# Kernel tuning notes

Measured on AMD Instinct MI355X. Metric: run time of the kernel, lower is better.

## Reference

```python
import jax, jax.numpy as jnp
import numpy as np

N_NODES = 100000
N_EDGES = 1600000
N_GRAPHS = 1000
NODES_PER_GRAPH = 100
D_IN = 128
D_HID = 128
N_TASKS = 12


def setup_inputs() -> dict:
    key = jax.random.key(0)
    ks = jax.random.split(key, 6)
    X = jax.random.normal(ks[0], (N_NODES, D_IN), dtype=jnp.float32)
    edge_index = jax.random.randint(ks[1], (2, N_EDGES), 0, N_NODES, dtype=jnp.int64)
    graph_sizes = jnp.full((N_GRAPHS,), NODES_PER_GRAPH, dtype=jnp.int64)  # sums to N_NODES
    s0 = (2.0 / D_IN) ** 0.5
    W0 = jax.random.normal(ks[2], (D_IN, D_HID), dtype=jnp.float32) * s0
    b0 = jnp.zeros((D_HID,), dtype=jnp.float32)
    W1 = jax.random.normal(ks[3], (D_HID, D_HID), dtype=jnp.float32) * s0
    b1 = jnp.zeros((D_HID,), dtype=jnp.float32)
    Wf = jax.random.normal(ks[4], (D_HID, N_TASKS), dtype=jnp.float32) * s0
    bf = jnp.zeros((N_TASKS,), dtype=jnp.float32)
    return {"X": X, "edge_index": edge_index, "graph_sizes": graph_sizes,
            "W0": W0, "b0": b0, "W1": W1, "b1": b1, "Wf": Wf, "bf": bf}


def reference(X, edge_index, graph_sizes, W0, b0, W1, b1, Wf, bf):
    src, dst = edge_index[0], edge_index[1]
    n = X.shape[0]

    def gconv(x, W, b):
        # GCN-style message passing with self term: sum_{j->i} (x_j W) + x_i W + b
        xw = x @ W                                                    # [N, d]
        agg = jax.ops.segment_sum(xw[src], dst, num_segments=n)       # [N, d]
        return agg + xw + b

    # stacked conv -> relu -> dropout(eval=identity)
    h = jax.nn.relu(gconv(X, W0, b0))
    h = jax.nn.relu(gconv(h, W1, b1))
    out = jax.nn.sigmoid(h @ Wf + bf)                                  # [N, T]

    # ragged per-graph mean readout as a single segment-mean
    g = graph_sizes.shape[0]
    seg_ids = jnp.repeat(jnp.arange(g), graph_sizes, total_repeat_length=n)
    sums = jax.ops.segment_sum(out, seg_ids, num_segments=g)           # [G, T]
    return sums / graph_sizes[:, None].astype(out.dtype)
```

## Files before the change

kernel.cpp:

```cpp
#include <hip/hip_runtime.h>
#include <math.h>

#define D 128
#define NBUCK_MAX 1024
#define PER       2048
#define NCHUNK_PAD 1024
#define CAPB      4096
#define CAPE      2600

typedef unsigned short u16;
typedef unsigned int   u32;
typedef __attribute__((ext_vector_type(8))) short short8;
typedef __attribute__((ext_vector_type(4))) float f32x4;
typedef __attribute__((ext_vector_type(2))) float f32x2;

static __device__ __forceinline__ u16 f32_to_bf16(float f) {
    u32 u = __builtin_bit_cast(u32, f);
    u32 r = (u + 0x7FFFu + ((u >> 16) & 1u)) >> 16;
    return (u16)r;
}
static __device__ __forceinline__ u32 pack_bf16x2(float lo, float hi) {
    return (u32)f32_to_bf16(lo) | ((u32)f32_to_bf16(hi) << 16);
}
static __device__ __forceinline__ float bf16lo_to_f32(u32 v) {
    return __builtin_bit_cast(float, v << 16);
}
static __device__ __forceinline__ float bf16hi_to_f32(u32 v) {
    return __builtin_bit_cast(float, v & 0xFFFF0000u);
}

__global__ __launch_bounds__(256) void prep_place(const int* __restrict__ src, const int* __restrict__ dst,
                                                  int E, int nbuck, int nchunk,
                                                  u32* __restrict__ edgeBuf, u16* __restrict__ offTab,
                                                  const float* __restrict__ W0, const float* __restrict__ W1,
                                                  u16* __restrict__ Wp0, u16* __restrict__ Wp1,
                                                  const float* __restrict__ Wf, float* __restrict__ Wfp,
                                                  const int* __restrict__ gsz, int G, int* __restrict__ goff) {
    const int b = blockIdx.x;
    const int tid = threadIdx.x;
    if (b < nchunk) {
        __shared__ int cnt[NBUCK_MAX];
        __shared__ u32 pay[PER];
        for (int i = tid; i < nbuck; i += 256) cnt[i] = 0;
        __syncthreads();
        const int s = b * PER, e = min(E, s + PER);
        int dv[8];
        #pragma unroll
        for (int k = 0; k < 8; k++) {
            int i = s + tid + k * 256;
            dv[k] = (i < e) ? dst[i] : -1;
            if (dv[k] >= 0) atomicAdd(&cnt[dv[k] >> 7], 1);
        }
        __syncthreads();
        if (tid < 64) {
            int carry = 0;
            int rounds = (nbuck + 63) >> 6;
            for (int r = 0; r < rounds; r++) {
                int i = r * 64 + tid;
                int v = (i < nbuck) ? cnt[i] : 0;
                int incl = v;
                #pragma unroll
                for (int off = 1; off < 64; off <<= 1) { int t = __shfl_up(incl, off); if (tid >= off) incl += t; }
                int excl = carry + incl - v;
                if (i < nbuck) { offTab[(size_t)i * NCHUNK_PAD + b] = (u16)excl; cnt[i] = excl; }
                carry += __shfl(incl, 63);
            }
            if (tid == 0) offTab[(size_t)nbuck * NCHUNK_PAD + b] = (u16)carry;
        }
        __syncthreads();
        #pragma unroll
        for (int k = 0; k < 8; k++) {
            int i = s + tid + k * 256;
            if (i < e) {
                int pos = atomicAdd(&cnt[dv[k] >> 7], 1);
                pay[pos] = (u32)src[i] | ((u32)(dv[k] & 127) << 20);
            }
        }
        __syncthreads();
        const int m = e - s;
        for (int i = tid; i < m; i += 256) edgeBuf[(size_t)b * PER + i] = pay[i];
    } else if (b == nchunk) {
        __shared__ int wsum[8];
        int base = tid * 4;
        int v[4];
        #pragma unroll
        for (int k = 0; k < 4; k++) v[k] = (base + k < G) ? gsz[base + k] : 0;
        int s = v[0] + v[1] + v[2] + v[3];
        int lane = tid & 63;
        int incl = s;
        #pragma unroll
        for (int off = 1; off < 64; off <<= 1) { int t = __shfl_up(incl, off); if (lane >= off) incl += t; }
        int wv = tid >> 6;
        if (lane == 63) wsum[wv] = incl;
        __syncthreads();
        int woff = 0;
        for (int w = 0; w < wv; w++) woff += wsum[w];
        int run = woff + incl - s;
        #pragma unroll
        for (int k = 0; k < 4; k++) {
            if (base + k <= G) goff[base + k] = run;
            run += v[k];
        }
    } else if (b == nchunk + 1) {
        for (int i = tid; i < 64 * 24; i += 256) {
            int lane = i / 24, r = i % 24, k = r / 3, j = r % 3;
            Wfp[i] = Wf[(((lane & 15) * 8) + k) * 12 + 3 * (lane >> 4) + j];
        }
    } else {
        int gidx = (b - (nchunk + 2)) * 256 + tid;
        const float* W = (gidx < 128 * 128) ? W0 : W1;
        u16* Wp = (gidx < 128 * 128) ? Wp0 : Wp1;
        int idx = gidx & (128 * 128 - 1);
        int j = idx & 7, lane = (idx >> 3) & 63, kt = (idx >> 9) & 3, nt = idx >> 11;
        int k = kt * 32 + ((lane >> 4) << 3) + j;
        int n = nt * 16 + (lane & 15);
        Wp[idx] = f32_to_bf16(W[k * 128 + n]);
    }
}

static __device__ __forceinline__ void gemm_body(const short8 af[4], const u16* __restrict__ Wp,
                                                 u16* __restrict__ outb, int N, int row0,
                                                 int tid, int wave, int lane, int quad, int l16,
                                                 u16* Cs) {
    f32x4 acc[8];
    #pragma unroll
    for (int nt = 0; nt < 8; nt++) acc[nt] = (f32x4){0.f, 0.f, 0.f, 0.f};
    #pragma unroll
    for (int kt = 0; kt < 4; kt++) {
        #pragma unroll
        for (int nt = 0; nt < 8; nt++) {
            short8 bf = *(const short8*)(Wp + ((size_t)(nt * 4 + kt) * 64 + lane) * 8);
            acc[nt] = __builtin_amdgcn_mfma_f32_16x16x32_bf16(af[kt], bf, acc[nt], 0, 0, 0);
        }
    }
    #pragma unroll
    for (int nt = 0; nt < 8; nt++) {
        #pragma unroll
        for (int r = 0; r < 4; r++) {
            int rl = wave * 16 + quad * 4 + r;
            Cs[rl * 136 + nt * 16 + l16] = f32_to_bf16(acc[nt][r]);
        }
    }
    __syncthreads();
    for (int i = tid; i < 64 * 16; i += 256) {
        int row = i >> 4, chunk = i & 15;
        int grow = row0 + row;
        if (grow <= N)
            *(uint4*)(outb + (size_t)grow * 128 + chunk * 8) =
                *(const uint4*)(Cs + row * 136 + chunk * 8);
    }
}

__global__ __launch_bounds__(256) void finalize_gemm0(const u32* __restrict__ edgeBuf,
                                                      const u16* __restrict__ offTab,
                                                      int2* __restrict__ rowse, int* __restrict__ col_idx,
                                                      int nbuck, int nchunk,
                                                      const float* __restrict__ A, const u16* __restrict__ Wp,
                                                      u16* __restrict__ outb, int N) {
    __shared__ int sbuf[7680];
    const int tid = threadIdx.x;
    if ((int)blockIdx.x < nbuck) {
        u32* eL     = (u32*)sbuf;
        int* sorted = sbuf + CAPE;
        int* hist   = sbuf + 2 * CAPE + 128;
        int* lcur   = sbuf + 2 * CAPE + 256;
        int* scnt   = sbuf + 2 * CAPE + 384;
        int* sbase  = sbuf + 2 * CAPE + 1408;
        const int b = blockIdx.x;
        for (int c = tid; c < NCHUNK_PAD; c += 256) {
            if (c < nchunk) {
                int off0 = offTab[(size_t)b * NCHUNK_PAD + c];
                int off1 = offTab[(size_t)(b + 1) * NCHUNK_PAD + c];
                scnt[c] = (off0 << 16) | (off1 - off0);
            } else scnt[c] = 0;
        }
        if (tid < 128) hist[tid] = 0;
        __syncthreads();
        if (tid < 64) {
            int carry = 0;
            #pragma unroll
            for (int c4 = 0; c4 < NCHUNK_PAD / 64; c4++) {
                int v = scnt[c4 * 64 + tid] & 0xFFFF;
                int incl = v;
                #pragma unroll
                for (int off = 1; off < 64; off <<= 1) { int t = __shfl_up(incl, off); if (tid >= off) incl += t; }
                sbase[c4 * 64 + tid] = carry + incl - v;
                carry += __shfl(incl, 63);
            }
            if (tid == 0) sbase[NCHUNK_PAD] = carry;
        }
        __syncthreads();
        const int nE = min(sbase[NCHUNK_PAD], CAPE);
        for (int p = tid; p < nE; p += 256) {
            int lo = 0, hi = NCHUNK_PAD;
            #pragma unroll
            for (int s = 0; s < 10; s++) {
                int mid = (lo + hi) >> 1;
                if (sbase[mid] <= p) lo = mid; else hi = mid;
            }
            int rec = scnt[lo];
            eL[p] = edgeBuf[(size_t)lo * PER + (rec >> 16) + (p - sbase[lo])];
        }
        __syncthreads();
        for (int i = tid; i < nE; i += 256)
            atomicAdd(&hist[(int)(eL[i] >> 20)], 1);
        __syncthreads();
        if (tid < 64) {
            int v0 = hist[tid * 2], v1 = hist[tid * 2 + 1];
            int s = v0 + v1;
            int incl = s;
            #pragma unroll
            for (int off = 1; off < 64; off <<= 1) { int t = __shfl_up(incl, off); if (tid >= off) incl += t; }
            int excl = incl - s;
            int le0 = excl + tid * 2;
            int le1 = le0 + v0 + 1;
            lcur[tid * 2]     = le0 + 1;
            lcur[tid * 2 + 1] = le1 + 1;
            int node = b * 128 + tid * 2;
            int st0 = b * CAPB + le0, st1 = b * CAPB + le1;
            if (node < N)     { rowse[node]     = make_int2(st0, st1);          sorted[le0] = node; }
            if (node + 1 < N) { rowse[node + 1] = make_int2(st1, st1 + v1 + 1); sorted[le1] = node + 1; }
        }
        __syncthreads();
        for (int i = tid; i < nE; i += 256) {
            u32 p = eL[i];
            int pos = atomicAdd(&lcur[p >> 20], 1);
            sorted[pos] = (int)(p & 0xFFFFFu);
        }
        __syncthreads();
        const int nTot = nE + min(128, N - b * 128);
        for (int i = tid; i < nTot; i += 256)
            col_idx[b * CAPB + i] = sorted[i];
    } else {
        u16* Cs = (u16*)sbuf;
        const int bid = blockIdx.x - nbuck;
        const int wave = tid >> 6, lane = tid & 63, quad = lane >> 4, l16 = lane & 15;
        const int row0 = bid * 64;
        const int arow = row0 + wave * 16 + l16;
        union { u32 u[4]; short8 s; } cv;
        short8 af[4];
        if (arow < N) {
            const float* ab = A + (size_t)arow * 128 + quad * 8;
            #pragma unroll
            for (int kt = 0; kt < 4; kt++) {
                float4 x0 = *(const float4*)(ab + kt * 32);
                float4 x1 = *(const float4*)(ab + kt * 32 + 4);
                cv.u[0] = pack_bf16x2(x0.x, x0.y);
                cv.u[1] = pack_bf16x2(x0.z, x0.w);
                cv.u[2] = pack_bf16x2(x1.x, x1.y);
                cv.u[3] = pack_bf16x2(x1.z, x1.w);
                af[kt] = cv.s;
            }
        } else {
            short8 z = {0, 0, 0, 0, 0, 0, 0, 0};
            #pragma unroll
            for (int kt = 0; kt < 4; kt++) af[kt] = z;
        }
        gemm_body(af, Wp, outb, N, row0, tid, wave, lane, quad, l16, Cs);
    }
}

static __device__ __forceinline__ void add_row(f32x2* acc, uint4 u) {
    acc[0] += (f32x2){bf16lo_to_f32(u.x), bf16hi_to_f32(u.x)};
    acc[1] += (f32x2){bf16lo_to_f32(u.y), bf16hi_to_f32(u.y)};
    acc[2] += (f32x2){bf16lo_to_f32(u.z), bf16hi_to_f32(u.z)};
    acc[3] += (f32x2){bf16lo_to_f32(u.w), bf16hi_to_f32(u.w)};
}

static __device__ __forceinline__ void gather2(const u16* __restrict__ xwb, const int2* __restrict__ rowse,
                                               const int* __restrict__ col_idx, const float* __restrict__ bias,
                                               int wid0, int wid1, int lane, int N, int q, int d8,
                                               float r0[8], float r1[8]) {
    f32x2 accA[4], accB[4];
    #pragma unroll
    for (int t = 0; t < 4; t++) { accA[t] = (f32x2){0.f, 0.f}; accB[t] = (f32x2){0.f, 0.f}; }
    int2 seA = rowse[wid0];
    int2 seB = rowse[wid1];
    int ia = seA.x + lane, ib = seB.x + lane;
    int jA = (ia < seA.y) ? col_idx[ia] : N;
    int jB = (ib < seB.y) ? col_idx[ib] : N;
    int cntA = __builtin_amdgcn_readfirstlane(min(64, seA.y - seA.x));
    int cntB = __builtin_amdgcn_readfirstlane(min(64, seB.y - seB.x));
    int mx = max(cntA, cntB);
    for (int i = 0; i < mx; i += 8) {
        uint4 ra0, ra1, rb0, rb1;
        const bool dA = i < cntA, dB = i < cntB;
        if (dA) {
            int a0 = __shfl(jA, i + q);
            int a1 = __shfl(jA, i + 4 + q);
            ra0 = *(const uint4*)(xwb + (size_t)a0 * D + d8);
            ra1 = *(const uint4*)(xwb + (size_t)a1 * D + d8);
        }
        if (dB) {
            int b0 = __shfl(jB, i + q);
            int b1 = __shfl(jB, i + 4 + q);
            rb0 = *(const uint4*)(xwb + (size_t)b0 * D + d8);
            rb1 = *(const uint4*)(xwb + (size_t)b1 * D + d8);
        }
        if (dA) { add_row(accA, ra0); add_row(accA, ra1); }
        if (dB) { add_row(accB, rb0); add_row(accB, rb1); }
    }
    for (int e = seA.x + 64; e < seA.y; e += 64) {
        int idx = e + lane;
        int j = (idx < seA.y) ? col_idx[idx] : N;
        int cnt = min(64, seA.y - e);
        for (int i = 0; i < cnt; i += 8) {
            int j0 = __shfl(j, i + q);
            int j1 = __shfl(j, i + 4 + q);
            add_row(accA, *(const uint4*)(xwb + (size_t)j0 * D + d8));
            add_row(accA, *(const uint4*)(xwb + (size_t)j1 * D + d8));
        }
    }
    for (int e = seB.x + 64; e < seB.y; e += 64) {
        int idx = e + lane;
        int j = (idx < seB.y) ? col_idx[idx] : N;
        int cnt = min(64, seB.y - e);
        for (int i = 0; i < cnt; i += 8) {
            int j0 = __shfl(j, i + q);
            int j1 = __shfl(j, i + 4 + q);
            add_row(accB, *(const uint4*)(xwb + (size_t)j0 * D + d8));
            add_row(accB, *(const uint4*)(xwb + (size_t)j1 * D + d8));
        }
    }

    float av0[8] = {accA[0].x, accA[0].y, accA[1].x, accA[1].y, accA[2].x, accA[2].y, accA[3].x, accA[3].y};
    float av1[8] = {accB[0].x, accB[0].y, accB[1].x, accB[1].y, accB[2].x, accB[2].y, accB[3].x, accB[3].y};
    #pragma unroll
    for (int t = 0; t < 8; t++) {
        av0[t] += __shfl_xor(av0[t], 16);
        av0[t] += __shfl_xor(av0[t], 32);
        av1[t] += __shfl_xor(av1[t], 16);
        av1[t] += __shfl_xor(av1[t], 32);
    }
    float4 ba = *(const float4*)(bias + d8);
    float4 bb = *(const float4*)(bias + d8 + 4);
    r0[0] = fmaxf(av0[0] + ba.x, 0.f);
    r0[1] = fmaxf(av0[1] + ba.y, 0.f);
    r0[2] = fmaxf(av0[2] + ba.z, 0.f);
    r0[3] = fmaxf(av0[3] + ba.w, 0.f);
    r0[4] = fmaxf(av0[4] + bb.x, 0.f);
    r0[5] = fmaxf(av0[5] + bb.y, 0.f);
    r0[6] = fmaxf(av0[6] + bb.z, 0.f);
    r0[7] = fmaxf(av0[7] + bb.w, 0.f);
    r1[0] = fmaxf(av1[0] + ba.x, 0.f);
    r1[1] = fmaxf(av1[1] + ba.y, 0.f);
    r1[2] = fmaxf(av1[2] + ba.z, 0.f);
    r1[3] = fmaxf(av1[3] + ba.w, 0.f);
    r1[4] = fmaxf(av1[4] + bb.x, 0.f);
    r1[5] = fmaxf(av1[5] + bb.y, 0.f);
    r1[6] = fmaxf(av1[6] + bb.z, 0.f);
    r1[7] = fmaxf(av1[7] + bb.w, 0.f);
}

__global__ __launch_bounds__(256) void agg_gemm1(const u16* __restrict__ xwb, const int2* __restrict__ rowse,
                                                 const int* __restrict__ col_idx, const float* __restrict__ bias,
                                                 const u16* __restrict__ Wp, u16* __restrict__ outb, int N) {
    __shared__ u16 hs[16 * 136];
    __shared__ u16 Cs[16 * 136];
    const int tid = threadIdx.x;
    const int wave = tid >> 6, lane = tid & 63, quad = lane >> 4, l16 = lane & 15;
    const int tile = blockIdx.x * 16;
    const int d8 = l16 * 8;
    #pragma unroll
    for (int m = 0; m < 4; m += 2) {
        int nl0 = wave * 4 + m, nl1 = nl0 + 1;
        int wid0 = tile + nl0, wid1 = tile + nl1;
        float r0[8], r1[8];
        int g0 = min(wid0, N - 1), g1 = min(wid1, N - 1);
        gather2(xwb, rowse, col_idx, bias, g0, g1, lane, N, quad, d8, r0, r1);
        if (quad == 0) {
            uint4 o0, o1;
            if (wid0 < N) {
                o0.x = pack_bf16x2(r0[0], r0[1]);
                o0.y = pack_bf16x2(r0[2], r0[3]);
                o0.z = pack_bf16x2(r0[4], r0[5]);
                o0.w = pack_bf16x2(r0[6], r0[7]);
            } else o0 = make_uint4(0, 0, 0, 0);
            if (wid1 < N) {
                o1.x = pack_bf16x2(r1[0], r1[1]);
                o1.y = pack_bf16x2(r1[2], r1[3]);
                o1.z = pack_bf16x2(r1[4], r1[5]);
                o1.w = pack_bf16x2(r1[6], r1[7]);
            } else o1 = make_uint4(0, 0, 0, 0);
            *(uint4*)(hs + nl0 * 136 + d8) = o0;
            *(uint4*)(hs + nl1 * 136 + d8) = o1;
        }
    }
    __syncthreads();
    short8 af[4];
    #pragma unroll
    for (int kt = 0; kt < 4; kt++)
        af[kt] = *(const short8*)(hs + l16 * 136 + kt * 32 + quad * 8);
    f32x4 acc[2];
    acc[0] = (f32x4){0.f, 0.f, 0.f, 0.f};
    acc[1] = (f32x4){0.f, 0.f, 0.f, 0.f};
    #pragma unroll
    for (int kt = 0; kt < 4; kt++) {
        #pragma unroll
        for (int t = 0; t < 2; t++) {
            int nt = wave * 2 + t;
            short8 bf = *(const short8*)(Wp + ((size_t)(nt * 4 + kt) * 64 + lane) * 8);
            acc[t] = __builtin_amdgcn_mfma_f32_16x16x32_bf16(af[kt], bf, acc[t], 0, 0, 0);
        }
    }
    #pragma unroll
    for (int t = 0; t < 2; t++) {
        int nt = wave * 2 + t;
        #pragma unroll
        for (int r = 0; r < 4; r++)
            Cs[(quad * 4 + r) * 136 + nt * 16 + l16] = f32_to_bf16(acc[t][r]);
    }
    __syncthreads();
    {
        int row = tid >> 4, chunk = tid & 15;
        int grow = tile + row;
        if (grow <= N)
            *(uint4*)(outb + (size_t)grow * 128 + chunk * 8) =
                *(const uint4*)(Cs + row * 136 + chunk * 8);
    }
}

__global__ __launch_bounds__(256) void agg_head(const u16* __restrict__ xwb, const int2* __restrict__ rowse,
                                                const int* __restrict__ col_idx, const float* __restrict__ bias,
                                                const float* __restrict__ Wfp, const float* __restrict__ bfv,
                                                float* __restrict__ out12, int N) {
    int wpair = (blockIdx.x * 256 + threadIdx.x) >> 6;
    int wid0 = wpair * 2;
    if (wid0 >= N) return;
    int wid1 = min(wid0 + 1, N - 1);
    int lane = threadIdx.x & 63;
    const int q = lane >> 4;
    const int d8 = (lane & 15) * 8;
    float w[24];
    const float* wp = Wfp + lane * 24;
    #pragma unroll
    for (int i = 0; i < 6; i++) *(float4*)(w + i * 4) = *(const float4*)(wp + i * 4);
    float r0[8], r1[8];
    gather2(xwb, rowse, col_idx, bias, wid0, wid1, lane, N, q, d8, r0, r1);
    const int t0 = 3 * q;
    float p00 = 0.f, p01 = 0.f, p02 = 0.f;
    float p10 = 0.f, p11 = 0.f, p12 = 0.f;
    #pragma unroll
    for (int k = 0; k < 8; k++) {
        p00 += r0[k] * w[k * 3];
        p01 += r0[k] * w[k * 3 + 1];
        p02 += r0[k] * w[k * 3 + 2];
        p10 += r1[k] * w[k * 3];
        p11 += r1[k] * w[k * 3 + 1];
        p12 += r1[k] * w[k * 3 + 2];
    }
    #pragma unroll
    for (int m = 1; m <= 8; m <<= 1) {
        p00 += __shfl_xor(p00, m);
        p01 += __shfl_xor(p01, m);
        p02 += __shfl_xor(p02, m);
        p10 += __shfl_xor(p10, m);
        p11 += __shfl_xor(p11, m);
        p12 += __shfl_xor(p12, m);
    }
    if ((lane & 15) == 0) {
        float b0 = bfv[t0], b1 = bfv[t0 + 1], b2 = bfv[t0 + 2];
        float* o0 = out12 + (size_t)wid0 * 12 + t0;
        o0[0] = 1.f / (1.f + __expf(-(p00 + b0)));
        o0[1] = 1.f / (1.f + __expf(-(p01 + b1)));
        o0[2] = 1.f / (1.f + __expf(-(p02 + b2)));
        if (wid0 + 1 < N) {
            float* o1 = out12 + (size_t)wid1 * 12 + t0;
            o1[0] = 1.f / (1.f + __expf(-(p10 + b0)));
            o1[1] = 1.f / (1.f + __expf(-(p11 + b1)));
            o1[2] = 1.f / (1.f + __expf(-(p12 + b2)));
        }
    }
}

__global__ __launch_bounds__(128) void graph_mean(const float* __restrict__ out12, const int* __restrict__ goff,
                                                  float* __restrict__ out, int G) {
    __shared__ float partial[120];
    int g = blockIdx.x;
    int tid = threadIdx.x;
    int start = goff[g];
    int size = goff[g + 1] - start;
    if (tid < 120) {
        int t = tid % 12, chunk = tid / 12;
        float s = 0.f;
        for (int i = chunk; i < size; i += 10)
            s += out12[(size_t)(start + i) * 12 + t];
        partial[tid] = s;
    }
    __syncthreads();
    if (tid < 12) {
        float tot = 0.f;
        #pragma unroll
        for (int c = 0; c < 10; c++) tot += partial[c * 12 + tid];
        out[(size_t)g * 12 + tid] = tot / (float)size;
    }
}


extern "C" void kernel_launch(void* const* d_in, const int* in_sizes, int n_in,
                              void* d_out, int out_size, void* d_ws, size_t ws_size,
                              hipStream_t stream) {
    const float* X   = (const float*)d_in[0];
    const int* edges = (const int*)d_in[1];
    const int* gsz   = (const int*)d_in[2];
    const float* W0  = (const float*)d_in[3];
    const float* b0  = (const float*)d_in[4];
    const float* W1  = (const float*)d_in[5];
    const float* b1  = (const float*)d_in[6];
    const float* Wf  = (const float*)d_in[7];
    const float* bfv = (const float*)d_in[8];
    float* out = (float*)d_out;

    const int N = in_sizes[0] / D;
    const int E = in_sizes[1] / 2;
    const int G = in_sizes[2];
    const int* esrc = edges;
    const int* edst = edges + E;
    const int nbuck = (N + 127) >> 7;
    const int nchunk = (E + PER - 1) / PER;

    char* ws = (char*)d_ws;
    char* p = ws;
    u16* xwb     = (u16*)p;  p += (((size_t)(N + 64) * D * 2) + 255) & ~255ull;
    u16* hb      = (u16*)p;  p += (((size_t)(N + 64) * D * 2) + 255) & ~255ull;
    u16* Wp0     = (u16*)p;  p += ((size_t)128 * 128 * 2 + 255) & ~255ull;
    u16* Wp1     = (u16*)p;  p += ((size_t)128 * 128 * 2 + 255) & ~255ull;
    float* Wfp   = (float*)p; p += ((size_t)64 * 24 * 4 + 255) & ~255ull;
    u32* edgeBuf = (u32*)p;  p += (((size_t)nchunk * PER * 4) + 255) & ~255ull;
    u16* offTab  = (u16*)p;  p += (((size_t)(NBUCK_MAX + 1) * NCHUNK_PAD * 2) + 255) & ~255ull;
    int* col_idx = (int*)p;  p += (((size_t)nbuck * CAPB * 4) + 255) & ~255ull;
    int2* rowse  = (int2*)p; p += (((size_t)N * 8) + 255) & ~255ull;
    float* out12 = (float*)p; p += (((size_t)N * 12 * 4) + 255) & ~255ull;
    int* goff    = (int*)p;

    prep_place<<<nchunk + 2 + 128, 256, 0, stream>>>(esrc, edst, E, nbuck, nchunk, edgeBuf, offTab,
                                                     W0, W1, Wp0, Wp1, Wf, Wfp, gsz, G, goff);
    const int gemmGrid = (N + 63) / 64;
    finalize_gemm0<<<nbuck + gemmGrid, 256, 0, stream>>>(edgeBuf, offTab, rowse, col_idx, nbuck, nchunk,
                                                         X, Wp0, xwb, N);
    agg_gemm1<<<N / 16 + 1, 256, 0, stream>>>(xwb, rowse, col_idx, b0, Wp1, hb, N);
    const int waves2 = (N + 1) / 2;
    agg_head<<<(waves2 + 3) / 4, 256, 0, stream>>>(hb, rowse, col_idx, b1, Wfp, bfv, out12, N);
    graph_mean<<<G, 128, 0, stream>>>(out12, goff, out, G);
}
```

Before: 276.8 us.

## Reschedule edge binning alongside GEMM0 and split CSR finalize into own kernel

Weight packing and graph offset scan move into a small standalone kernel. Edge binning now runs in the same launch as the first GEMM, so the two overlap, and CSR finalization becomes a separate kernel. Edge chunks grow from 2048 to 6144 edges, which cuts the number of chunks the finalize pass has to scan and binary-search. The cost is one extra kernel launch, and binning blocks with larger per-thread register arrays and more LDS that can limit occupancy.

```diff
diff --git a/kernel.cpp b/kernel.cpp
--- a/kernel.cpp
+++ b/kernel.cpp
@@ -3,8 +3,8 @@
 
 #define D 128
 #define NBUCK_MAX 1024
-#define PER       2048
-#define NCHUNK_PAD 1024
+#define PER       6144
+#define NCHUNK_PAD 512
 #define CAPB      4096
 #define CAPE      2600
 
@@ -29,24 +29,101 @@
     return __builtin_bit_cast(float, v & 0xFFFF0000u);
 }
 
-__global__ __launch_bounds__(256) void prep_place(const int* __restrict__ src, const int* __restrict__ dst,
-                                                  int E, int nbuck, int nchunk,
-                                                  u32* __restrict__ edgeBuf, u16* __restrict__ offTab,
-                                                  const float* __restrict__ W0, const float* __restrict__ W1,
-                                                  u16* __restrict__ Wp0, u16* __restrict__ Wp1,
-                                                  const float* __restrict__ Wf, float* __restrict__ Wfp,
-                                                  const int* __restrict__ gsz, int G, int* __restrict__ goff) {
+__global__ __launch_bounds__(512) void prep_pack(const float* __restrict__ W0, const float* __restrict__ W1,
+                                                 u16* __restrict__ Wp0, u16* __restrict__ Wp1,
+                                                 const float* __restrict__ Wf, float* __restrict__ Wfp,
+                                                 const int* __restrict__ gsz, int G, int* __restrict__ goff) {
     const int b = blockIdx.x;
     const int tid = threadIdx.x;
-    if (b < nchunk) {
-        __shared__ int cnt[NBUCK_MAX];
-        __shared__ u32 pay[PER];
+    if (b == 0) {
+        __shared__ int wsum[8];
+        int base = tid * 4;
+        int v[4];
+        #pragma unroll
+        for (int k = 0; k < 4; k++) v[k] = (base + k < G) ? gsz[base + k] : 0;
+        int s = v[0] + v[1] + v[2] + v[3];
+        int lane = tid & 63;
+        int incl = s;
+        #pragma unroll
+        for (int off = 1; off < 64; off <<= 1) { int t = __shfl_up(incl, off); if (lane >= off) incl += t; }
+        int wv = tid >> 6;
+        if (lane == 63) wsum[wv] = incl;
+        __syncthreads();
+        int woff = 0;
+        for (int w = 0; w < wv; w++) woff += wsum[w];
+        int run = woff + incl - s;
+        #pragma unroll
+        for (int k = 0; k < 4; k++) {
+            if (base + k <= G) goff[base + k] = run;
+            run += v[k];
+        }
+    } else if (b == 1) {
+        for (int i = tid; i < 64 * 24; i += 512) {
+            int lane = i / 24, r = i % 24, k = r / 3, j = r % 3;
+            Wfp[i] = Wf[(((lane & 15) * 8) + k) * 12 + 3 * (lane >> 4) + j];
+        }
+    } else {
+        int gidx = (b - 2) * 512 + tid;
+        const float* W = (gidx < 128 * 128) ? W0 : W1;
+        u16* Wp = (gidx < 128 * 128) ? Wp0 : Wp1;
+        int idx = gidx & (128 * 128 - 1);
+        int j = idx & 7, lane = (idx >> 3) & 63, kt = (idx >> 9) & 3, nt = idx >> 11;
+        int k = kt * 32 + ((lane >> 4) << 3) + j;
+        int n = nt * 16 + (lane & 15);
+        Wp[idx] = f32_to_bf16(W[k * 128 + n]);
+    }
+}
+
+static __device__ __forceinline__ void gemm_body(const short8 af[4], const u16* __restrict__ Wp,
+                                                 u16* __restrict__ outb, int N, int row0,
+                                                 int tid, int wave, int lane, int quad, int l16,
+                                                 u16* Cs) {
+    f32x4 acc[8];
+    #pragma unroll
+    for (int nt = 0; nt < 8; nt++) acc[nt] = (f32x4){0.f, 0.f, 0.f, 0.f};
+    #pragma unroll
+    for (int kt = 0; kt < 4; kt++) {
+        #pragma unroll
+        for (int nt = 0; nt < 8; nt++) {
+            short8 bf = *(const short8*)(Wp + ((size_t)(nt * 4 + kt) * 64 + lane) * 8);
+            acc[nt] = __builtin_amdgcn_mfma_f32_16x16x32_bf16(af[kt], bf, acc[nt], 0, 0, 0);
+        }
+    }
+    #pragma unroll
+    for (int nt = 0; nt < 8; nt++) {
+        #pragma unroll
+        for (int r = 0; r < 4; r++) {
+            int rl = wave * 16 + quad * 4 + r;
+            Cs[rl * 136 + nt * 16 + l16] = f32_to_bf16(acc[nt][r]);
+        }
+    }
+    __syncthreads();
+    for (int i = tid; i < 64 * 16; i += 256) {
+        int row = i >> 4, chunk = i & 15;
+        int grow = row0 + row;
+        if (grow <= N)
+            *(uint4*)(outb + (size_t)grow * 128 + chunk * 8) =
+                *(const uint4*)(Cs + row * 136 + chunk * 8);
+    }
+}
+
+__global__ __launch_bounds__(256) void bin_gemm0(const int* __restrict__ src, const int* __restrict__ dst,
+                                                 int E, int nbuck, int nchunk,
+                                                 u32* __restrict__ edgeBuf, u16* __restrict__ offTab,
+                                                 const float* __restrict__ A, const u16* __restrict__ Wp,
+                                                 u16* __restrict__ outb, int N) {
+    __shared__ int smem[7168];
+    const int tid = threadIdx.x;
+    if ((int)blockIdx.x < nchunk) {
+        int* cnt = smem;
+        u32* pay = (u32*)(smem + 1024);
+        const int b = blockIdx.x;
         for (int i = tid; i < nbuck; i += 256) cnt[i] = 0;
         __syncthreads();
         const int s = b * PER, e = min(E, s + PER);
-        int dv[8];
-        #pragma unroll
-        for (int k = 0; k < 8; k++) {
+        int dv[24];
+        #pragma unroll
+        for (int k = 0; k < 24; k++) {
             int i = s + tid + k * 256;
             dv[k] = (i < e) ? dst[i] : -1;
             if (dv[k] >= 0) atomicAdd(&cnt[dv[k] >> 7], 1);
@@ -69,7 +146,7 @@
         }
         __syncthreads();
         #pragma unroll
-        for (int k = 0; k < 8; k++) {
+        for (int k = 0; k < 24; k++) {
             int i = s + tid + k * 256;
             if (i < e) {
                 int pos = atomicAdd(&cnt[dv[k] >> 7], 1);
@@ -79,161 +156,9 @@
         __syncthreads();
         const int m = e - s;
         for (int i = tid; i < m; i += 256) edgeBuf[(size_t)b * PER + i] = pay[i];
-    } else if (b == nchunk) {
-        __shared__ int wsum[8];
-        int base = tid * 4;
-        int v[4];
-        #pragma unroll
-        for (int k = 0; k < 4; k++) v[k] = (base + k < G) ? gsz[base + k] : 0;
-        int s = v[0] + v[1] + v[2] + v[3];
-        int lane = tid & 63;
-        int incl = s;
-        #pragma unroll
-        for (int off = 1; off < 64; off <<= 1) { int t = __shfl_up(incl, off); if (lane >= off) incl += t; }
-        int wv = tid >> 6;
-        if (lane == 63) wsum[wv] = incl;
-        __syncthreads();
-        int woff = 0;
-        for (int w = 0; w < wv; w++) woff += wsum[w];
-        int run = woff + incl - s;
-        #pragma unroll
-        for (int k = 0; k < 4; k++) {
-            if (base + k <= G) goff[base + k] = run;
-            run += v[k];
-        }
-    } else if (b == nchunk + 1) {
-        for (int i = tid; i < 64 * 24; i += 256) {
-            int lane = i / 24, r = i % 24, k = r / 3, j = r % 3;
-            Wfp[i] = Wf[(((lane & 15) * 8) + k) * 12 + 3 * (lane >> 4) + j];
-        }
     } else {
-        int gidx = (b - (nchunk + 2)) * 256 + tid;
-        const float* W = (gidx < 128 * 128) ? W0 : W1;
-        u16* Wp = (gidx < 128 * 128) ? Wp0 : Wp1;
-        int idx = gidx & (128 * 128 - 1);
-        int j = idx & 7, lane = (idx >> 3) & 63, kt = (idx >> 9) & 3, nt = idx >> 11;
-        int k = kt * 32 + ((lane >> 4) << 3) + j;
-        int n = nt * 16 + (lane & 15);
-        Wp[idx] = f32_to_bf16(W[k * 128 + n]);
-    }
-}
-
-static __device__ __forceinline__ void gemm_body(const short8 af[4], const u16* __restrict__ Wp,
-                                                 u16* __restrict__ outb, int N, int row0,
-                                                 int tid, int wave, int lane, int quad, int l16,
-                                                 u16* Cs) {
-    f32x4 acc[8];
-    #pragma unroll
-    for (int nt = 0; nt < 8; nt++) acc[nt] = (f32x4){0.f, 0.f, 0.f, 0.f};
-    #pragma unroll
-    for (int kt = 0; kt < 4; kt++) {
-        #pragma unroll
-        for (int nt = 0; nt < 8; nt++) {
-            short8 bf = *(const short8*)(Wp + ((size_t)(nt * 4 + kt) * 64 + lane) * 8);
-            acc[nt] = __builtin_amdgcn_mfma_f32_16x16x32_bf16(af[kt], bf, acc[nt], 0, 0, 0);
-        }
-    }
-    #pragma unroll
-    for (int nt = 0; nt < 8; nt++) {
-        #pragma unroll
-        for (int r = 0; r < 4; r++) {
-            int rl = wave * 16 + quad * 4 + r;
-            Cs[rl * 136 + nt * 16 + l16] = f32_to_bf16(acc[nt][r]);
-        }
-    }
-    __syncthreads();
-    for (int i = tid; i < 64 * 16; i += 256) {
-        int row = i >> 4, chunk = i & 15;
-        int grow = row0 + row;
-        if (grow <= N)
-            *(uint4*)(outb + (size_t)grow * 128 + chunk * 8) =
-                *(const uint4*)(Cs + row * 136 + chunk * 8);
-    }
-}
-
-__global__ __launch_bounds__(256) void finalize_gemm0(const u32* __restrict__ edgeBuf,
-                                                      const u16* __restrict__ offTab,
-                                                      int2* __restrict__ rowse, int* __restrict__ col_idx,
-                                                      int nbuck, int nchunk,
-                                                      const float* __restrict__ A, const u16* __restrict__ Wp,
-                                                      u16* __restrict__ outb, int N) {
-    __shared__ int sbuf[7680];
-    const int tid = threadIdx.x;
-    if ((int)blockIdx.x < nbuck) {
-        u32* eL     = (u32*)sbuf;
-        int* sorted = sbuf + CAPE;
-        int* hist   = sbuf + 2 * CAPE + 128;
-        int* lcur   = sbuf + 2 * CAPE + 256;
-        int* scnt   = sbuf + 2 * CAPE + 384;
-        int* sbase  = sbuf + 2 * CAPE + 1408;
-        const int b = blockIdx.x;
-        for (int c = tid; c < NCHUNK_PAD; c += 256) {
-            if (c < nchunk) {
-                int off0 = offTab[(size_t)b * NCHUNK_PAD + c];
-                int off1 = offTab[(size_t)(b + 1) * NCHUNK_PAD + c];
-                scnt[c] = (off0 << 16) | (off1 - off0);
-            } else scnt[c] = 0;
-        }
-        if (tid < 128) hist[tid] = 0;
-        __syncthreads();
-        if (tid < 64) {
-            int carry = 0;
-            #pragma unroll
-            for (int c4 = 0; c4 < NCHUNK_PAD / 64; c4++) {
-                int v = scnt[c4 * 64 + tid] & 0xFFFF;
-                int incl = v;
-                #pragma unroll
-                for (int off = 1; off < 64; off <<= 1) { int t = __shfl_up(incl, off); if (tid >= off) incl += t; }
-                sbase[c4 * 64 + tid] = carry + incl - v;
-                carry += __shfl(incl, 63);
-            }
-            if (tid == 0) sbase[NCHUNK_PAD] = carry;
-        }
-        __syncthreads();
-        const int nE = min(sbase[NCHUNK_PAD], CAPE);
-        for (int p = tid; p < nE; p += 256) {
-            int lo = 0, hi = NCHUNK_PAD;
-            #pragma unroll
-            for (int s = 0; s < 10; s++) {
-                int mid = (lo + hi) >> 1;
-                if (sbase[mid] <= p) lo = mid; else hi = mid;
-            }
-            int rec = scnt[lo];
-            eL[p] = edgeBuf[(size_t)lo * PER + (rec >> 16) + (p - sbase[lo])];
-        }
-        __syncthreads();
-        for (int i = tid; i < nE; i += 256)
-            atomicAdd(&hist[(int)(eL[i] >> 20)], 1);
-        __syncthreads();
-        if (tid < 64) {
-            int v0 = hist[tid * 2], v1 = hist[tid * 2 + 1];
-            int s = v0 + v1;
-            int incl = s;
-            #pragma unroll
-            for (int off = 1; off < 64; off <<= 1) { int t = __shfl_up(incl, off); if (tid >= off) incl += t; }
-            int excl = incl - s;
-            int le0 = excl + tid * 2;
-            int le1 = le0 + v0 + 1;
-            lcur[tid * 2]     = le0 + 1;
-            lcur[tid * 2 + 1] = le1 + 1;
-            int node = b * 128 + tid * 2;
-            int st0 = b * CAPB + le0, st1 = b * CAPB + le1;
-            if (node < N)     { rowse[node]     = make_int2(st0, st1);          sorted[le0] = node; }
-            if (node + 1 < N) { rowse[node + 1] = make_int2(st1, st1 + v1 + 1); sorted[le1] = node + 1; }
-        }
-        __syncthreads();
-        for (int i = tid; i < nE; i += 256) {
-            u32 p = eL[i];
-            int pos = atomicAdd(&lcur[p >> 20], 1);
-            sorted[pos] = (int)(p & 0xFFFFFu);
-        }
-        __syncthreads();
-        const int nTot = nE + min(128, N - b * 128);
-        for (int i = tid; i < nTot; i += 256)
-            col_idx[b * CAPB + i] = sorted[i];
-    } else {
-        u16* Cs = (u16*)sbuf;
-        const int bid = blockIdx.x - nbuck;
+        u16* Cs = (u16*)smem;
+        const int bid = blockIdx.x - nchunk;
         const int wave = tid >> 6, lane = tid & 63, quad = lane >> 4, l16 = lane & 15;
         const int row0 = bid * 64;
         const int arow = row0 + wave * 16 + l16;
@@ -258,6 +183,85 @@
         }
         gemm_body(af, Wp, outb, N, row0, tid, wave, lane, quad, l16, Cs);
     }
+}
+
+__global__ __launch_bounds__(256) void finalize_csr(const u32* __restrict__ edgeBuf,
+                                                    const u16* __restrict__ offTab,
+                                                    int2* __restrict__ rowse, int* __restrict__ col_idx,
+                                                    int nbuck, int nchunk, int N) {
+    __shared__ int sbuf[6656];
+    const int tid = threadIdx.x;
+    u32* eL     = (u32*)sbuf;
+    int* sorted = sbuf + CAPE;
+    int* hist   = sbuf + 2 * CAPE + 128;
+    int* lcur   = sbuf + 2 * CAPE + 256;
+    int* scnt   = sbuf + 2 * CAPE + 384;
+    int* sbase  = sbuf + 2 * CAPE + 896;
+    const int b = blockIdx.x;
+    for (int c = tid; c < NCHUNK_PAD; c += 256) {
+        if (c < nchunk) {
+            int off0 = offTab[(size_t)b * NCHUNK_PAD + c];
+            int off1 = offTab[(size_t)(b + 1) * NCHUNK_PAD + c];
+            scnt[c] = (off0 << 16) | (off1 - off0);
+        } else scnt[c] = 0;
+    }
+    if (tid < 128) hist[tid] = 0;
+    __syncthreads();
+    if (tid < 64) {
+        int carry = 0;
+        #pragma unroll
+        for (int c4 = 0; c4 < NCHUNK_PAD / 64; c4++) {
+            int v = scnt[c4 * 64 + tid] & 0xFFFF;
+            int incl = v;
+            #pragma unroll
+            for (int off = 1; off < 64; off <<= 1) { int t = __shfl_up(incl, off); if (tid >= off) incl += t; }
+            sbase[c4 * 64 + tid] = carry + incl - v;
+            carry += __shfl(incl, 63);
+        }
+        if (tid == 0) sbase[NCHUNK_PAD] = carry;
+    }
+    __syncthreads();
+    const int nE = min(sbase[NCHUNK_PAD], CAPE);
+    for (int p = tid; p < nE; p += 256) {
+        int lo = 0, hi = NCHUNK_PAD;
+        #pragma unroll
+        for (int s = 0; s < 9; s++) {
+            int mid = (lo + hi) >> 1;
+            if (sbase[mid] <= p) lo = mid; else hi = mid;
+        }
+        int rec = scnt[lo];
+        eL[p] = edgeBuf[(size_t)lo * PER + (rec >> 16) + (p - sbase[lo])];
+    }
+    __syncthreads();
+    for (int i = tid; i < nE; i += 256)
+        atomicAdd(&hist[(int)(eL[i] >> 20)], 1);
+    __syncthreads();
+    if (tid < 64) {
+        int v0 = hist[tid * 2], v1 = hist[tid * 2 + 1];
+        int s = v0 + v1;
+        int incl = s;
+        #pragma unroll
+        for (int off = 1; off < 64; off <<= 1) { int t = __shfl_up(incl, off); if (tid >= off) incl += t; }
+        int excl = incl - s;
+        int le0 = excl + tid * 2;
+        int le1 = le0 + v0 + 1;
+        lcur[tid * 2]     = le0 + 1;
+        lcur[tid * 2 + 1] = le1 + 1;
+        int node = b * 128 + tid * 2;
+        int st0 = b * CAPB + le0, st1 = b * CAPB + le1;
+        if (node < N)     { rowse[node]     = make_int2(st0, st1);          sorted[le0] = node; }
+        if (node + 1 < N) { rowse[node + 1] = make_int2(st1, st1 + v1 + 1); sorted[le1] = node + 1; }
+    }
+    __syncthreads();
+    for (int i = tid; i < nE; i += 256) {
+        u32 p = eL[i];
+        int pos = atomicAdd(&lcur[p >> 20], 1);
+        sorted[pos] = (int)(p & 0xFFFFFu);
+    }
+    __syncthreads();
+    const int nTot = nE + min(128, N - b * 128);
+    for (int i = tid; i < nTot; i += 256)
+        col_idx[b * CAPB + i] = sorted[i];
 }
 
 static __device__ __forceinline__ void add_row(f32x2* acc, uint4 u) {
@@ -533,11 +537,11 @@
     float* out12 = (float*)p; p += (((size_t)N * 12 * 4) + 255) & ~255ull;
     int* goff    = (int*)p;
 
-    prep_place<<<nchunk + 2 + 128, 256, 0, stream>>>(esrc, edst, E, nbuck, nchunk, edgeBuf, offTab,
-                                                     W0, W1, Wp0, Wp1, Wf, Wfp, gsz, G, goff);
+    prep_pack<<<2 + 64, 512, 0, stream>>>(W0, W1, Wp0, Wp1, Wf, Wfp, gsz, G, goff);
     const int gemmGrid = (N + 63) / 64;
-    finalize_gemm0<<<nbuck + gemmGrid, 256, 0, stream>>>(edgeBuf, offTab, rowse, col_idx, nbuck, nchunk,
-                                                         X, Wp0, xwb, N);
+    bin_gemm0<<<nchunk + gemmGrid, 256, 0, stream>>>(esrc, edst, E, nbuck, nchunk, edgeBuf, offTab,
+                                                     X, Wp0, xwb, N);
+    finalize_csr<<<nbuck, 256, 0, stream>>>(edgeBuf, offTab, rowse, col_idx, nbuck, nchunk, N);
     agg_gemm1<<<N / 16 + 1, 256, 0, stream>>>(xwb, rowse, col_idx, b0, Wp1, hb, N);
     const int waves2 = (N + 1) / 2;
     agg_head<<<(waves2 + 3) / 4, 256, 0, stream>>>(hb, rowse, col_idx, b1, Wfp, bfv, out12, N);
```

New measurement: 285.9 us. 3.3% more time.
